# Optimization experiments

Measured on AMD Instinct MI355X. Metric: run time of the kernel, lower is better.

The kernel has to match this reference:

```python
import jax, jax.numpy as jnp
import numpy as np

N_NODES = 50000
N_EDGES = 600000
NUM_GRAPHS = 64


def gcn_conv(x, W, b, src, dst, n):
    # PyG GCNConv: x' = D^{-1/2} (A + I) D^{-1/2} (x W) + b, self-loops implicit
    h = x @ W  # [N, H]
    deg = jax.ops.segment_sum(jnp.ones((src.shape[0],), h.dtype), dst, num_segments=n) + 1.0
    dinv = jax.lax.rsqrt(deg)  # [N]
    norm = dinv[src] * dinv[dst]  # [E]
    msg = h[src] * norm[:, None]  # [E, H] gather + scale
    agg = jax.ops.segment_sum(msg, dst, num_segments=n)  # scatter-add
    agg = agg + h * (dinv * dinv)[:, None]  # self-loop contribution
    return agg + b


def global_mean_pool(x, batch, num_graphs):
    s = jax.ops.segment_sum(x, batch, num_segments=num_graphs)
    cnt = jax.ops.segment_sum(jnp.ones((x.shape[0],), x.dtype), batch, num_segments=num_graphs)
    return s / jnp.maximum(cnt, 1.0)[:, None]


def setup_inputs() -> dict:
    key = jax.random.key(0)
    ks = jax.random.split(key, 12)
    x = jax.random.normal(ks[0], (N_NODES, 128), jnp.float32)
    edge_index = jax.random.randint(ks[1], (2, N_EDGES), 0, N_NODES, jnp.int64)
    batch = jnp.sort(jax.random.randint(ks[2], (N_NODES,), 0, NUM_GRAPHS, jnp.int64))
    W1 = jax.random.normal(ks[3], (128, 128), jnp.float32) * 0.08
    b1 = jax.random.normal(ks[4], (128,), jnp.float32) * 0.02
    W2 = jax.random.normal(ks[5], (128, 128), jnp.float32) * 0.08
    b2 = jax.random.normal(ks[6], (128,), jnp.float32) * 0.02
    Wfc1 = jax.random.normal(ks[7], (128, 64), jnp.float32) * 0.08
    bfc1 = jax.random.normal(ks[8], (64,), jnp.float32) * 0.02
    Wfc2 = jax.random.normal(ks[9], (64, 1), jnp.float32) * 0.08
    bfc2 = jax.random.normal(ks[10], (1,), jnp.float32) * 0.02
    return {"x": x, "edge_index": edge_index, "batch": batch,
            "W1": W1, "b1": b1, "W2": W2, "b2": b2,
            "Wfc1": Wfc1, "bfc1": bfc1, "Wfc2": Wfc2, "bfc2": bfc2}


def reference(x, edge_index, batch, W1, b1, W2, b2, Wfc1, bfc1, Wfc2, bfc2):
    n = x.shape[0]
    src, dst = edge_index[0], edge_index[1]
    h = jax.nn.relu(gcn_conv(x, W1, b1, src, dst, n))
    # dropout = identity (eval mode)
    h = jax.nn.relu(gcn_conv(h, W2, b2, src, dst, n))
    g = global_mean_pool(h, batch, NUM_GRAPHS)  # [G, H]
    g = jax.nn.relu(g @ Wfc1 + bfc1)
    return g @ Wfc2 + bfc2  # [G, 1]
```

## Files before the change

### kernel.cpp

```cpp
#include <hip/hip_runtime.h>
#include <hip/hip_fp16.h>


#define ELLK 48

typedef short bf16x8 __attribute__((ext_vector_type(8)));
typedef float f32x4  __attribute__((ext_vector_type(4)));

__device__ inline unsigned short f2bf_rne(float f) {
    unsigned u = __float_as_uint(f);
    unsigned r = (u + 0x7fffu + ((u >> 16) & 1u)) >> 16;
    return (unsigned short)r;
}
__device__ inline float bf2f(unsigned short h) {
    return __uint_as_float(((unsigned)h) << 16);
}

__global__ __launch_bounds__(256) void wconv_zero(const float* __restrict__ W1,
                                                  const float* __restrict__ W2,
                                                  unsigned short* __restrict__ W1h,
                                                  unsigned short* __restrict__ W1l,
                                                  unsigned short* __restrict__ W2h,
                                                  unsigned short* __restrict__ W2l,
                                                  int* __restrict__ count,
                                                  float* __restrict__ pooled,
                                                  float* __restrict__ cnt, int N) {
    int tid = threadIdx.x;
    int b = blockIdx.x;
    if (b < 128) {
        int i = b * 256 + tid;
        const float* W = (i < 16384) ? W1 : W2;
        unsigned short* Wh = (i < 16384) ? W1h : W2h;
        unsigned short* Wl = (i < 16384) ? W1l : W2l;
        int ii = i & 16383;
        int k = ii >> 7, n = ii & 127;
        float v = W[ii];
        unsigned short h = f2bf_rne(v);
        float lo = v - bf2f(h);
        int ct = n >> 4, nn = n & 15, ks = k >> 5, q = (k >> 3) & 3, j = k & 7;
        int oidx = (((ct * 4 + ks) * 64) + (q * 16 + nn)) * 8 + j;
        Wh[oidx] = h;
        Wl[oidx] = f2bf_rne(lo);
    } else {
        int idx = (b - 128) * 256 + tid;
        if (idx < N) count[idx] = 0;
        else if (idx < N + 8192) pooled[idx - N] = 0.f;
        else if (idx < N + 8256) cnt[idx - N - 8192] = 0.f;
    }
}

template <bool RELU_IN>
__device__ __forceinline__ void gemm_body(const float* __restrict__ X,
                                          const unsigned short* __restrict__ Wfh,
                                          const unsigned short* __restrict__ Wfl,
                                          __half* __restrict__ OUT, int M, int blk) {
    __shared__ unsigned short Xh[64][136];
    __shared__ unsigned short Xl[64][136];
    int tid = threadIdx.x;
    int w = tid >> 6, l = tid & 63;
    int m0 = blk * 64;

#pragma unroll
    for (int it = 0; it < 8; it++) {
        int i = tid + it * 256;
        int row = i >> 5, c4 = i & 31;
        int grow = m0 + row;
        float4 v = make_float4(0.f, 0.f, 0.f, 0.f);
        if (grow < M) v = *(const float4*)(X + (size_t)grow * 128 + c4 * 4);
        if (RELU_IN) {
            v.x = fmaxf(v.x, 0.f); v.y = fmaxf(v.y, 0.f);
            v.z = fmaxf(v.z, 0.f); v.w = fmaxf(v.w, 0.f);
        }
        float a[4] = {v.x, v.y, v.z, v.w};
        ushort4 hi, lo;
        unsigned short* hp = (unsigned short*)&hi;
        unsigned short* lp = (unsigned short*)&lo;
#pragma unroll
        for (int e = 0; e < 4; e++) {
            unsigned short h = f2bf_rne(a[e]);
            hp[e] = h;
            lp[e] = f2bf_rne(a[e] - bf2f(h));
        }
        *(ushort4*)&Xh[row][c4 * 4] = hi;
        *(ushort4*)&Xl[row][c4 * 4] = lo;
    }
    __syncthreads();

    int q = l >> 4, nn = l & 15;
    f32x4 acc[8];
#pragma unroll
    for (int ct = 0; ct < 8; ct++) acc[ct] = (f32x4){0.f, 0.f, 0.f, 0.f};

#pragma unroll
    for (int ks = 0; ks < 4; ks++) {
        bf16x8 ahi = *(const bf16x8*)&Xh[w * 16 + nn][ks * 32 + q * 8];
        bf16x8 alo = *(const bf16x8*)&Xl[w * 16 + nn][ks * 32 + q * 8];
#pragma unroll
        for (int ct = 0; ct < 8; ct++) {
            size_t fo = ((size_t)(ct * 4 + ks) * 64 + l) * 8;
            bf16x8 bhi = *(const bf16x8*)(Wfh + fo);
            bf16x8 blo = *(const bf16x8*)(Wfl + fo);
            acc[ct] = __builtin_amdgcn_mfma_f32_16x16x32_bf16(ahi, bhi, acc[ct], 0, 0, 0);
            acc[ct] = __builtin_amdgcn_mfma_f32_16x16x32_bf16(alo, bhi, acc[ct], 0, 0, 0);
            acc[ct] = __builtin_amdgcn_mfma_f32_16x16x32_bf16(ahi, blo, acc[ct], 0, 0, 0);
        }
    }
    __syncthreads();

#pragma unroll
    for (int r = 0; r < 4; r++) {
        int lrow = w * 16 + q * 4 + r;
#pragma unroll
        for (int ct = 0; ct < 8; ct++) {
            __half hv = __float2half(acc[ct][r]);
            Xh[lrow][ct * 16 + nn] = __half_as_ushort(hv);
        }
    }
    __syncthreads();
#pragma unroll
    for (int t = 0; t < 4; t++) {
        int c = tid + t * 256;
        int row = c >> 4, seg = c & 15;
        int grow = m0 + row;
        if (grow < M) {
            uint4 v = *(uint4*)&Xh[row][seg * 8];
            *(uint4*)((unsigned short*)OUT + (size_t)grow * 128 + seg * 8) = v;
        }
    }
}

__global__ __launch_bounds__(256) void fused_hg(const float* __restrict__ X,
                                                const unsigned short* __restrict__ Wfh,
                                                const unsigned short* __restrict__ Wfl,
                                                __half* __restrict__ OUT, int M, int gblocks,
                                                const int* __restrict__ dst,
                                                int* __restrict__ count,
                                                unsigned short* __restrict__ rank, int E) {
    if ((int)blockIdx.x < gblocks) {
        gemm_body<false>(X, Wfh, Wfl, OUT, M, blockIdx.x);
    } else {
        int e = ((int)blockIdx.x - gblocks) * 256 + (int)threadIdx.x;
        if (e < E) {
            int d = dst[e];
            rank[e] = (unsigned short)atomicAdd(&count[d], 1);
        }
    }
}

__global__ void scatter_norm(const int* __restrict__ src, const int* __restrict__ dst,
                             const unsigned short* __restrict__ rank,
                             const int* __restrict__ count,
                             int2* __restrict__ ell, int E, int N, int hb) {
    int b = blockIdx.x;
    if (b < hb) {
        int e = b * 256 + (int)threadIdx.x;
        if (e < E) {
            int s = src[e], d = dst[e];
            int r = rank[e];
            float ds = 1.0f / sqrtf((float)count[s] + 1.0f);
            float dd = 1.0f / sqrtf((float)count[d] + 1.0f);
            if (r < ELLK) ell[(size_t)d * ELLK + r] = make_int2(s, __float_as_int(ds * dd));
        }
    } else {
        int n = (b - hb) * 256 + (int)threadIdx.x;
        if (n < N) {
            int r = min(count[n], ELLK);
            int rend = min(ELLK, max(16, (r + 15) & ~15));
            int2 z = make_int2(0, 0);
            for (int j = r; j < rend; j++) ell[(size_t)n * ELLK + j] = z;
        }
    }
}

__device__ __forceinline__ void fma8(const uint4& raw, float nr, float a[8]) {
    const __half2* hh = (const __half2*)&raw;
    float2 f0 = __half22float2(hh[0]), f1 = __half22float2(hh[1]);
    float2 f2 = __half22float2(hh[2]), f3 = __half22float2(hh[3]);
    a[0] = fmaf(f0.x, nr, a[0]); a[1] = fmaf(f0.y, nr, a[1]);
    a[2] = fmaf(f1.x, nr, a[2]); a[3] = fmaf(f1.y, nr, a[3]);
    a[4] = fmaf(f2.x, nr, a[4]); a[5] = fmaf(f2.y, nr, a[5]);
    a[6] = fmaf(f3.x, nr, a[6]); a[7] = fmaf(f3.y, nr, a[7]);
}

__device__ __forceinline__ void gather_process(const unsigned short* __restrict__ hb,
                                               const long long* __restrict__ ell,
                                               int n, int sub, int cl,
                                               long long u0, long long u1,
                                               long long u2, long long u3,
                                               int cn, float a[8]) {
    uint4 r0 = *(const uint4*)(hb + (size_t)(int)u0 * 128 + cl * 8);
    uint4 r1 = *(const uint4*)(hb + (size_t)(int)u1 * 128 + cl * 8);
    uint4 r2 = *(const uint4*)(hb + (size_t)(int)u2 * 128 + cl * 8);
    uint4 r3 = *(const uint4*)(hb + (size_t)(int)u3 * 128 + cl * 8);
    float din = 1.0f / sqrtf((float)cn + 1.0f);
    if (sub == 0) {
        float sw = din * din;
        uint4 sr = *(const uint4*)(hb + (size_t)n * 128 + cl * 8);
        fma8(sr, sw, a);
    }
    fma8(r0, __int_as_float((int)(u0 >> 32)), a);
    fma8(r1, __int_as_float((int)(u1 >> 32)), a);
    fma8(r2, __int_as_float((int)(u2 >> 32)), a);
    fma8(r3, __int_as_float((int)(u3 >> 32)), a);
    int cle = min((min(cn, ELLK) + 15) & ~15, ELLK);
    for (int base = 16; base < cle; base += 16) {
        const long long* rp = ell + (size_t)n * ELLK + base;
        long long v0 = rp[sub], v1 = rp[sub + 4], v2 = rp[sub + 8], v3 = rp[sub + 12];
        uint4 q0 = *(const uint4*)(hb + (size_t)(int)v0 * 128 + cl * 8);
        uint4 q1 = *(const uint4*)(hb + (size_t)(int)v1 * 128 + cl * 8);
        uint4 q2 = *(const uint4*)(hb + (size_t)(int)v2 * 128 + cl * 8);
        uint4 q3 = *(const uint4*)(hb + (size_t)(int)v3 * 128 + cl * 8);
        fma8(q0, __int_as_float((int)(v0 >> 32)), a);
        fma8(q1, __int_as_float((int)(v1 >> 32)), a);
        fma8(q2, __int_as_float((int)(v2 >> 32)), a);
        fma8(q3, __int_as_float((int)(v3 >> 32)), a);
    }
}

__global__ __launch_bounds__(512) void gather_gemm(const __half* __restrict__ h,
                                                   const float* __restrict__ bias,
                                                   const int* __restrict__ count,
                                                   const long long* __restrict__ ell,
                                                   const unsigned short* __restrict__ Wfh,
                                                   const unsigned short* __restrict__ Wfl,
                                                   __half* __restrict__ OUT, int N) {
    __shared__ unsigned short Xh[64][136];
    __shared__ unsigned short Xl[64][136];
    int tid = threadIdx.x;
    int w = tid >> 6, l = tid & 63;
    int sub = l >> 4, cl = l & 15;
    int m0 = blockIdx.x * 64;
    const unsigned short* hb = (const unsigned short*)h;

    {
        int ncur = min(m0 + w * 8, N - 1);
        const long long* rp = ell + (size_t)ncur * ELLK;
        long long u0 = rp[sub], u1 = rp[sub + 4], u2 = rp[sub + 8], u3 = rp[sub + 12];
        int ccur = count[ncur];
        for (int rr = 0; rr < 8; rr++) {
            int n = m0 + w * 8 + rr;
            int ne = min(n, N - 1);
            long long v0 = 0, v1 = 0, v2 = 0, v3 = 0;
            int cnx = 0;
            if (rr < 7) {
                int nn = min(ne + 1, N - 1);
                const long long* rq = ell + (size_t)nn * ELLK;
                v0 = rq[sub]; v1 = rq[sub + 4]; v2 = rq[sub + 8]; v3 = rq[sub + 12];
                cnx = count[nn];
            }
            float a[8] = {0.f, 0.f, 0.f, 0.f, 0.f, 0.f, 0.f, 0.f};
            gather_process(hb, ell, ne, sub, cl, u0, u1, u2, u3, ccur, a);
#pragma unroll
            for (int m = 16; m < 64; m <<= 1) {
#pragma unroll
                for (int k = 0; k < 8; k++) a[k] += __shfl_xor(a[k], m, 64);
            }
            if (sub == 0) {
                int lrow = w * 8 + rr;
                unsigned short hs[8], ls[8];
#pragma unroll
                for (int k = 0; k < 8; k++) {
                    float vv = fmaxf(a[k] + bias[cl * 8 + k], 0.f);
                    unsigned short hh = f2bf_rne(vv);
                    hs[k] = hh;
                    ls[k] = f2bf_rne(vv - bf2f(hh));
                }
                *(ushort4*)&Xh[lrow][cl * 8]     = *(ushort4*)&hs[0];
                *(ushort4*)&Xh[lrow][cl * 8 + 4] = *(ushort4*)&hs[4];
                *(ushort4*)&Xl[lrow][cl * 8]     = *(ushort4*)&ls[0];
                *(ushort4*)&Xl[lrow][cl * 8 + 4] = *(ushort4*)&ls[4];
            }
            u0 = v0; u1 = v1; u2 = v2; u3 = v3; ccur = cnx;
        }
    }
    __syncthreads();

    int q = l >> 4, nn = l & 15;
    int w2 = w & 3;
    int ch = (w >> 2) * 4;
    f32x4 acc[4];
#pragma unroll
    for (int ct2 = 0; ct2 < 4; ct2++) acc[ct2] = (f32x4){0.f, 0.f, 0.f, 0.f};
#pragma unroll
    for (int ks = 0; ks < 4; ks++) {
        bf16x8 ahi = *(const bf16x8*)&Xh[w2 * 16 + nn][ks * 32 + q * 8];
        bf16x8 alo = *(const bf16x8*)&Xl[w2 * 16 + nn][ks * 32 + q * 8];
#pragma unroll
        for (int ct2 = 0; ct2 < 4; ct2++) {
            int ct = ch + ct2;
            size_t fo = ((size_t)(ct * 4 + ks) * 64 + l) * 8;
            bf16x8 bhi = *(const bf16x8*)(Wfh + fo);
            bf16x8 blo = *(const bf16x8*)(Wfl + fo);
            acc[ct2] = __builtin_amdgcn_mfma_f32_16x16x32_bf16(ahi, bhi, acc[ct2], 0, 0, 0);
            acc[ct2] = __builtin_amdgcn_mfma_f32_16x16x32_bf16(alo, bhi, acc[ct2], 0, 0, 0);
            acc[ct2] = __builtin_amdgcn_mfma_f32_16x16x32_bf16(ahi, blo, acc[ct2], 0, 0, 0);
        }
    }
    __syncthreads();
#pragma unroll
    for (int r = 0; r < 4; r++) {
        int lrow = w2 * 16 + q * 4 + r;
#pragma unroll
        for (int ct2 = 0; ct2 < 4; ct2++) {
            __half hv = __float2half(acc[ct2][r]);
            Xh[lrow][(ch + ct2) * 16 + nn] = __half_as_ushort(hv);
        }
    }
    __syncthreads();
#pragma unroll
    for (int t = 0; t < 2; t++) {
        int c = tid + t * 512;
        int row = c >> 4, seg = c & 15;
        int grow = m0 + row;
        if (grow < N) {
            uint4 v = *(uint4*)&Xh[row][seg * 8];
            *(uint4*)((unsigned short*)OUT + (size_t)grow * 128 + seg * 8) = v;
        }
    }
}

__global__ __launch_bounds__(512) void gather_pool(const __half* __restrict__ h,
                                                   const float* __restrict__ bias,
                                                   const int* __restrict__ count,
                                                   const long long* __restrict__ ell,
                                                   const int* __restrict__ batch,
                                                   float* __restrict__ pooled,
                                                   float* __restrict__ cnt, int N) {
    __shared__ float P[64][128];
    __shared__ int gb[64];
    int tid = threadIdx.x;
    int w = tid >> 6, l = tid & 63;
    int sub = l >> 4, cl = l & 15;
    int m0 = blockIdx.x * 64;
    const unsigned short* hb = (const unsigned short*)h;

    if (tid < 64) gb[tid] = (m0 + tid < N) ? batch[m0 + tid] : -1;

    {
        int ncur = min(m0 + w * 8, N - 1);
        const long long* rp = ell + (size_t)ncur * ELLK;
        long long u0 = rp[sub], u1 = rp[sub + 4], u2 = rp[sub + 8], u3 = rp[sub + 12];
        int ccur = count[ncur];
        for (int rr = 0; rr < 8; rr++) {
            int n = m0 + w * 8 + rr;
            int ne = min(n, N - 1);
            long long v0 = 0, v1 = 0, v2 = 0, v3 = 0;
            int cnx = 0;
            if (rr < 7) {
                int nn = min(ne + 1, N - 1);
                const long long* rq = ell + (size_t)nn * ELLK;
                v0 = rq[sub]; v1 = rq[sub + 4]; v2 = rq[sub + 8]; v3 = rq[sub + 12];
                cnx = count[nn];
            }
            float a[8] = {0.f, 0.f, 0.f, 0.f, 0.f, 0.f, 0.f, 0.f};
            gather_process(hb, ell, ne, sub, cl, u0, u1, u2, u3, ccur, a);
#pragma unroll
            for (int m = 16; m < 64; m <<= 1) {
#pragma unroll
                for (int k = 0; k < 8; k++) a[k] += __shfl_xor(a[k], m, 64);
            }
            if (sub == 0) {
                int lrow = w * 8 + rr;
#pragma unroll
                for (int k = 0; k < 8; k++)
                    P[lrow][cl * 8 + k] = fmaxf(a[k] + bias[cl * 8 + k], 0.f);
            }
            u0 = v0; u1 = v1; u2 = v2; u3 = v3; ccur = cnx;
        }
    }
    __syncthreads();

    int c = tid & 127, quarter = tid >> 7;
    float acc = 0.f, cacc = 0.f;
    int curg = -1;
    for (int i = quarter * 16; i < quarter * 16 + 16; i++) {
        int n = m0 + i;
        if (n >= N) break;
        int g = gb[i];
        float v = P[i][c];
        if (g != curg) {
            if (curg >= 0) {
                atomicAdd(&pooled[curg * 128 + c], acc);
                if (c == 0) atomicAdd(&cnt[curg], cacc);
            }
            curg = g; acc = 0.f; cacc = 0.f;
        }
        acc += v; cacc += 1.f;
    }
    if (curg >= 0) {
        atomicAdd(&pooled[curg * 128 + c], acc);
        if (c == 0) atomicAdd(&cnt[curg], cacc);
    }
}

__global__ __launch_bounds__(64) void head_kernel(const float* __restrict__ pooled,
                                                  const float* __restrict__ cnt,
                                                  const float* __restrict__ Wfc1,
                                                  const float* __restrict__ bfc1,
                                                  const float* __restrict__ Wfc2,
                                                  const float* __restrict__ bfc2,
                                                  float* __restrict__ out) {
    __shared__ float mean[128];
    int g = blockIdx.x;
    int t = threadIdx.x;
    float inv = 1.0f / fmaxf(cnt[g], 1.0f);
    mean[t] = pooled[g * 128 + t] * inv;
    mean[t + 64] = pooled[g * 128 + t + 64] * inv;
    __syncthreads();
    float s = bfc1[t];
#pragma unroll 4
    for (int k = 0; k < 128; k++) s = fmaf(mean[k], Wfc1[k * 64 + t], s);
    float p = fmaxf(s, 0.f) * Wfc2[t];
#pragma unroll
    for (int o = 32; o > 0; o >>= 1) p += __shfl_down(p, o, 64);
    if (t == 0) out[g] = p + bfc2[0];
}

extern "C" void kernel_launch(void* const* d_in, const int* in_sizes, int n_in,
                              void* d_out, int out_size, void* d_ws, size_t ws_size,
                              hipStream_t stream) {
    const float* x    = (const float*)d_in[0];
    const int*   edge = (const int*)d_in[1];
    const int*   batch= (const int*)d_in[2];
    const float* W1   = (const float*)d_in[3];
    const float* b1   = (const float*)d_in[4];
    const float* W2   = (const float*)d_in[5];
    const float* b2   = (const float*)d_in[6];
    const float* Wfc1 = (const float*)d_in[7];
    const float* bfc1 = (const float*)d_in[8];
    const float* Wfc2 = (const float*)d_in[9];
    const float* bfc2 = (const float*)d_in[10];
    float* out = (float*)d_out;

    int N = in_sizes[0] / 128;
    int E = in_sizes[1] / 2;
    const int* src = edge;
    const int* dst = edge + E;

    char* ws = (char*)d_ws;
    size_t off = 0;
    auto alloc = [&](size_t bytes) { void* p = ws + off; off += (bytes + 255) & ~(size_t)255; return p; };
    __half* Ah    = (__half*)alloc((size_t)N * 128 * sizeof(__half));
    __half* Ah2   = (__half*)alloc((size_t)N * 128 * sizeof(__half));
    int*   count  = (int*)alloc((size_t)N * sizeof(int));
    unsigned short* rank = (unsigned short*)alloc((size_t)E * sizeof(unsigned short));
    int2*  ell    = (int2*)alloc((size_t)N * ELLK * sizeof(int2));
    float* pooled = (float*)alloc(64 * 128 * sizeof(float));
    float* cnt    = (float*)alloc(64 * sizeof(float));
    unsigned short* W1h = (unsigned short*)alloc(16384 * sizeof(short));
    unsigned short* W1l = (unsigned short*)alloc(16384 * sizeof(short));
    unsigned short* W2h = (unsigned short*)alloc(16384 * sizeof(short));
    unsigned short* W2l = (unsigned short*)alloc(16384 * sizeof(short));

    int hb = (E + 255) / 256;
    int nzb = (N + 255) / 256;
    int gblocks = (N + 63) / 64;
    int fblocks = (N + 63) / 64;
    int zb = (N + 8256 + 255) / 256;

    wconv_zero<<<128 + zb, 256, 0, stream>>>(W1, W2, W1h, W1l, W2h, W2l,
                                             count, pooled, cnt, N);

    fused_hg<<<gblocks + hb, 256, 0, stream>>>(x, W1h, W1l, Ah, N, gblocks,
                                               dst, count, rank, E);

    scatter_norm<<<hb + nzb, 256, 0, stream>>>(src, dst, rank, count, ell, E, N, hb);

    gather_gemm<<<fblocks, 512, 0, stream>>>(Ah, b1, count, (const long long*)ell,
                                             W2h, W2l, Ah2, N);

    gather_pool<<<fblocks, 512, 0, stream>>>(Ah2, b2, count, (const long long*)ell,
                                             batch, pooled, cnt, N);

    head_kernel<<<64, 64, 0, stream>>>(pooled, cnt, Wfc1, bfc1, Wfc2, bfc2, out);
}
```

Baseline: 237.2 us.

## Stage ELL rows in shared memory and gather with 2 sub-lanes × 8 neighbors

Both gather kernels now preload the first 32 ELL entries per node of the 64-node tile into shared memory with a coalesced cooperative load. Each wave then processes a node with 2 sub-groups × 32 lanes reading 8-byte half chunks, issuing 8 independent row loads per lane to raise memory-level parallelism, and needs only one shuffle-reduction step. The pooling kernel also drops the shared P buffer and accumulates per-wave partial sums, which adds more atomics (8 waves per block instead of 4 quarters). The trade-off is narrower per-lane loads, extra LDS use, and a fixed 32-slot staging cost even for low-degree nodes.

```diff
diff --git a/kernel.cpp b/kernel.cpp
--- a/kernel.cpp
+++ b/kernel.cpp
@@ -172,48 +172,46 @@
     }
 }
 
-__device__ __forceinline__ void fma8(const uint4& raw, float nr, float a[8]) {
-    const __half2* hh = (const __half2*)&raw;
-    float2 f0 = __half22float2(hh[0]), f1 = __half22float2(hh[1]);
-    float2 f2 = __half22float2(hh[2]), f3 = __half22float2(hh[3]);
+__device__ __forceinline__ void fma4(uint2 raw, float nr, float a[4]) {
+    __half2 h0 = *(__half2*)&raw.x, h1 = *(__half2*)&raw.y;
+    float2 f0 = __half22float2(h0), f1 = __half22float2(h1);
     a[0] = fmaf(f0.x, nr, a[0]); a[1] = fmaf(f0.y, nr, a[1]);
     a[2] = fmaf(f1.x, nr, a[2]); a[3] = fmaf(f1.y, nr, a[3]);
-    a[4] = fmaf(f2.x, nr, a[4]); a[5] = fmaf(f2.y, nr, a[5]);
-    a[6] = fmaf(f3.x, nr, a[6]); a[7] = fmaf(f3.y, nr, a[7]);
-}
-
-__device__ __forceinline__ void gather_process(const unsigned short* __restrict__ hb,
-                                               const long long* __restrict__ ell,
-                                               int n, int sub, int cl,
-                                               long long u0, long long u1,
-                                               long long u2, long long u3,
-                                               int cn, float a[8]) {
-    uint4 r0 = *(const uint4*)(hb + (size_t)(int)u0 * 128 + cl * 8);
-    uint4 r1 = *(const uint4*)(hb + (size_t)(int)u1 * 128 + cl * 8);
-    uint4 r2 = *(const uint4*)(hb + (size_t)(int)u2 * 128 + cl * 8);
-    uint4 r3 = *(const uint4*)(hb + (size_t)(int)u3 * 128 + cl * 8);
+}
+
+__device__ __forceinline__ void gather_node8(const unsigned short* __restrict__ hb,
+                                             const long long* __restrict__ em_row,
+                                             const long long* __restrict__ ell_row,
+                                             int n, int cn, int sub2, int cl2,
+                                             float a[4]) {
+    int2 v[8];
+#pragma unroll
+    for (int k = 0; k < 8; k++) *(long long*)&v[k] = em_row[sub2 + k * 2];
     float din = 1.0f / sqrtf((float)cn + 1.0f);
-    if (sub == 0) {
-        float sw = din * din;
-        uint4 sr = *(const uint4*)(hb + (size_t)n * 128 + cl * 8);
-        fma8(sr, sw, a);
-    }
-    fma8(r0, __int_as_float((int)(u0 >> 32)), a);
-    fma8(r1, __int_as_float((int)(u1 >> 32)), a);
-    fma8(r2, __int_as_float((int)(u2 >> 32)), a);
-    fma8(r3, __int_as_float((int)(u3 >> 32)), a);
-    int cle = min((min(cn, ELLK) + 15) & ~15, ELLK);
-    for (int base = 16; base < cle; base += 16) {
-        const long long* rp = ell + (size_t)n * ELLK + base;
-        long long v0 = rp[sub], v1 = rp[sub + 4], v2 = rp[sub + 8], v3 = rp[sub + 12];
-        uint4 q0 = *(const uint4*)(hb + (size_t)(int)v0 * 128 + cl * 8);
-        uint4 q1 = *(const uint4*)(hb + (size_t)(int)v1 * 128 + cl * 8);
-        uint4 q2 = *(const uint4*)(hb + (size_t)(int)v2 * 128 + cl * 8);
-        uint4 q3 = *(const uint4*)(hb + (size_t)(int)v3 * 128 + cl * 8);
-        fma8(q0, __int_as_float((int)(v0 >> 32)), a);
-        fma8(q1, __int_as_float((int)(v1 >> 32)), a);
-        fma8(q2, __int_as_float((int)(v2 >> 32)), a);
-        fma8(q3, __int_as_float((int)(v3 >> 32)), a);
+    uint2 sr = *(const uint2*)(hb + (size_t)n * 128 + cl2 * 4);
+    uint2 r[8];
+#pragma unroll
+    for (int k = 0; k < 8; k++) r[k] = *(const uint2*)(hb + (size_t)v[k].x * 128 + cl2 * 4);
+    fma4(sr, sub2 == 0 ? din * din : 0.f, a);
+#pragma unroll
+    for (int k = 0; k < 8; k++) fma4(r[k], __int_as_float(v[k].y), a);
+    if (cn > 16) {
+        int2 u[8];
+#pragma unroll
+        for (int k = 0; k < 8; k++) *(long long*)&u[k] = em_row[16 + sub2 + k * 2];
+        uint2 q[8];
+#pragma unroll
+        for (int k = 0; k < 8; k++) q[k] = *(const uint2*)(hb + (size_t)u[k].x * 128 + cl2 * 4);
+#pragma unroll
+        for (int k = 0; k < 8; k++) fma4(q[k], __int_as_float(u[k].y), a);
+        if (cn > 32) {
+#pragma unroll
+            for (int k = 0; k < 8; k++) {
+                long long vv = ell_row[32 + sub2 + k * 2];
+                uint2 qq = *(const uint2*)(hb + (size_t)(int)vv * 128 + cl2 * 4);
+                fma4(qq, __int_as_float((int)(vv >> 32)), a);
+            }
+        }
     }
 }
 
@@ -224,53 +222,48 @@
                                                    const unsigned short* __restrict__ Wfh,
                                                    const unsigned short* __restrict__ Wfl,
                                                    __half* __restrict__ OUT, int N) {
+    __shared__ long long em_l[64 * 32];
+    __shared__ int cnt_l[64];
     __shared__ unsigned short Xh[64][136];
     __shared__ unsigned short Xl[64][136];
     int tid = threadIdx.x;
     int w = tid >> 6, l = tid & 63;
-    int sub = l >> 4, cl = l & 15;
+    int sub2 = l >> 5, cl2 = l & 31;
     int m0 = blockIdx.x * 64;
     const unsigned short* hb = (const unsigned short*)h;
 
-    {
-        int ncur = min(m0 + w * 8, N - 1);
-        const long long* rp = ell + (size_t)ncur * ELLK;
-        long long u0 = rp[sub], u1 = rp[sub + 4], u2 = rp[sub + 8], u3 = rp[sub + 12];
-        int ccur = count[ncur];
-        for (int rr = 0; rr < 8; rr++) {
-            int n = m0 + w * 8 + rr;
-            int ne = min(n, N - 1);
-            long long v0 = 0, v1 = 0, v2 = 0, v3 = 0;
-            int cnx = 0;
-            if (rr < 7) {
-                int nn = min(ne + 1, N - 1);
-                const long long* rq = ell + (size_t)nn * ELLK;
-                v0 = rq[sub]; v1 = rq[sub + 4]; v2 = rq[sub + 8]; v3 = rq[sub + 12];
-                cnx = count[nn];
+    for (int i = tid; i < 64 * 32; i += 512) {
+        int node = i >> 5, slot = i & 31;
+        int ne = min(m0 + node, N - 1);
+        em_l[i] = ell[(size_t)ne * ELLK + slot];
+    }
+    if (tid < 64) cnt_l[tid] = count[min(m0 + tid, N - 1)];
+    __syncthreads();
+
+    float b4[4];
+#pragma unroll
+    for (int k = 0; k < 4; k++) b4[k] = bias[cl2 * 4 + k];
+
+    for (int rr = 0; rr < 8; rr++) {
+        int lrow = w * 8 + rr;
+        int n = m0 + lrow;
+        int ne = min(n, N - 1);
+        float a[4] = {0.f, 0.f, 0.f, 0.f};
+        gather_node8(hb, em_l + lrow * 32, ell + (size_t)ne * ELLK,
+                     ne, cnt_l[lrow], sub2, cl2, a);
+#pragma unroll
+        for (int k = 0; k < 4; k++) a[k] += __shfl_xor(a[k], 32, 64);
+        if (sub2 == 0) {
+            unsigned short hs[4], ls[4];
+#pragma unroll
+            for (int k = 0; k < 4; k++) {
+                float vv = fmaxf(a[k] + b4[k], 0.f);
+                unsigned short hh = f2bf_rne(vv);
+                hs[k] = hh;
+                ls[k] = f2bf_rne(vv - bf2f(hh));
             }
-            float a[8] = {0.f, 0.f, 0.f, 0.f, 0.f, 0.f, 0.f, 0.f};
-            gather_process(hb, ell, ne, sub, cl, u0, u1, u2, u3, ccur, a);
-#pragma unroll
-            for (int m = 16; m < 64; m <<= 1) {
-#pragma unroll
-                for (int k = 0; k < 8; k++) a[k] += __shfl_xor(a[k], m, 64);
-            }
-            if (sub == 0) {
-                int lrow = w * 8 + rr;
-                unsigned short hs[8], ls[8];
-#pragma unroll
-                for (int k = 0; k < 8; k++) {
-                    float vv = fmaxf(a[k] + bias[cl * 8 + k], 0.f);
-                    unsigned short hh = f2bf_rne(vv);
-                    hs[k] = hh;
-                    ls[k] = f2bf_rne(vv - bf2f(hh));
-                }
-                *(ushort4*)&Xh[lrow][cl * 8]     = *(ushort4*)&hs[0];
-                *(ushort4*)&Xh[lrow][cl * 8 + 4] = *(ushort4*)&hs[4];
-                *(ushort4*)&Xl[lrow][cl * 8]     = *(ushort4*)&ls[0];
-                *(ushort4*)&Xl[lrow][cl * 8 + 4] = *(ushort4*)&ls[4];
-            }
-            u0 = v0; u1 = v1; u2 = v2; u3 = v3; ccur = cnx;
+            *(ushort4*)&Xh[lrow][cl2 * 4] = *(ushort4*)hs;
+            *(ushort4*)&Xl[lrow][cl2 * 4] = *(ushort4*)ls;
         }
     }
     __syncthreads();
@@ -326,70 +319,63 @@
                                                    const int* __restrict__ batch,
                                                    float* __restrict__ pooled,
                                                    float* __restrict__ cnt, int N) {
-    __shared__ float P[64][128];
-    __shared__ int gb[64];
+    __shared__ long long em_l[64 * 32];
+    __shared__ int cnt_l[64];
     int tid = threadIdx.x;
     int w = tid >> 6, l = tid & 63;
-    int sub = l >> 4, cl = l & 15;
+    int sub2 = l >> 5, cl2 = l & 31;
     int m0 = blockIdx.x * 64;
     const unsigned short* hb = (const unsigned short*)h;
 
-    if (tid < 64) gb[tid] = (m0 + tid < N) ? batch[m0 + tid] : -1;
-
-    {
-        int ncur = min(m0 + w * 8, N - 1);
-        const long long* rp = ell + (size_t)ncur * ELLK;
-        long long u0 = rp[sub], u1 = rp[sub + 4], u2 = rp[sub + 8], u3 = rp[sub + 12];
-        int ccur = count[ncur];
-        for (int rr = 0; rr < 8; rr++) {
-            int n = m0 + w * 8 + rr;
-            int ne = min(n, N - 1);
-            long long v0 = 0, v1 = 0, v2 = 0, v3 = 0;
-            int cnx = 0;
-            if (rr < 7) {
-                int nn = min(ne + 1, N - 1);
-                const long long* rq = ell + (size_t)nn * ELLK;
-                v0 = rq[sub]; v1 = rq[sub + 4]; v2 = rq[sub + 8]; v3 = rq[sub + 12];
-                cnx = count[nn];
-            }
-            float a[8] = {0.f, 0.f, 0.f, 0.f, 0.f, 0.f, 0.f, 0.f};
-            gather_process(hb, ell, ne, sub, cl, u0, u1, u2, u3, ccur, a);
-#pragma unroll
-            for (int m = 16; m < 64; m <<= 1) {
-#pragma unroll
-                for (int k = 0; k < 8; k++) a[k] += __shfl_xor(a[k], m, 64);
-            }
-            if (sub == 0) {
-                int lrow = w * 8 + rr;
-#pragma unroll
-                for (int k = 0; k < 8; k++)
-                    P[lrow][cl * 8 + k] = fmaxf(a[k] + bias[cl * 8 + k], 0.f);
-            }
-            u0 = v0; u1 = v1; u2 = v2; u3 = v3; ccur = cnx;
-        }
-    }
-    __syncthreads();
-
-    int c = tid & 127, quarter = tid >> 7;
-    float acc = 0.f, cacc = 0.f;
+    for (int i = tid; i < 64 * 32; i += 512) {
+        int node = i >> 5, slot = i & 31;
+        int ne = min(m0 + node, N - 1);
+        em_l[i] = ell[(size_t)ne * ELLK + slot];
+    }
+    if (tid < 64) cnt_l[tid] = count[min(m0 + tid, N - 1)];
+    __syncthreads();
+
+    float b4[4];
+#pragma unroll
+    for (int k = 0; k < 4; k++) b4[k] = bias[cl2 * 4 + k];
+
+    float pacc[4] = {0.f, 0.f, 0.f, 0.f};
+    float pcnt = 0.f;
     int curg = -1;
-    for (int i = quarter * 16; i < quarter * 16 + 16; i++) {
-        int n = m0 + i;
+    for (int rr = 0; rr < 8; rr++) {
+        int lrow = w * 8 + rr;
+        int n = m0 + lrow;
         if (n >= N) break;
-        int g = gb[i];
-        float v = P[i][c];
+        int g = batch[n];
         if (g != curg) {
             if (curg >= 0) {
-                atomicAdd(&pooled[curg * 128 + c], acc);
-                if (c == 0) atomicAdd(&cnt[curg], cacc);
+                if (sub2 == 0) {
+#pragma unroll
+                    for (int k = 0; k < 4; k++)
+                        atomicAdd(&pooled[curg * 128 + cl2 * 4 + k], pacc[k]);
+                }
+                if (l == 0) atomicAdd(&cnt[curg], pcnt);
             }
-            curg = g; acc = 0.f; cacc = 0.f;
-        }
-        acc += v; cacc += 1.f;
+            curg = g;
+            pacc[0] = pacc[1] = pacc[2] = pacc[3] = 0.f;
+            pcnt = 0.f;
+        }
+        float a[4] = {0.f, 0.f, 0.f, 0.f};
+        gather_node8(hb, em_l + lrow * 32, ell + (size_t)n * ELLK,
+                     n, cnt_l[lrow], sub2, cl2, a);
+#pragma unroll
+        for (int k = 0; k < 4; k++) a[k] += __shfl_xor(a[k], 32, 64);
+#pragma unroll
+        for (int k = 0; k < 4; k++) pacc[k] += fmaxf(a[k] + b4[k], 0.f);
+        pcnt += 1.f;
     }
     if (curg >= 0) {
-        atomicAdd(&pooled[curg * 128 + c], acc);
-        if (c == 0) atomicAdd(&cnt[curg], cacc);
+        if (sub2 == 0) {
+#pragma unroll
+            for (int k = 0; k < 4; k++)
+                atomicAdd(&pooled[curg * 128 + cl2 * 4 + k], pacc[k]);
+        }
+        if (l == 0) atomicAdd(&cnt[curg], pcnt);
     }
 }
 
```

Result: no change. 241.1 us (+1.7%).
